# Kernel tuning notes

Measured on AMD Instinct MI355X. Metric: run time of the kernel, lower is better.

## Reference

```python
import jax, jax.numpy as jnp
import numpy as np

SC = 30.0
M = 0.5
EPS = 1e-12  # F.normalize default eps


def _l2norm(x, axis):
    n = jnp.sqrt(jnp.sum(x * x, axis=axis, keepdims=True))
    return x / jnp.maximum(n, EPS)


def setup_inputs() -> dict:
    key = jax.random.key(0)
    k1, k2, k3, k4, k5 = jax.random.split(key, 5)
    n, in_f, out_f, books, words = 1024, 2048, 4096, 8, 256
    lw = in_f // books  # len_word = 256
    # xavier_uniform-ish scale for params
    w_lim = np.sqrt(6.0 / (out_f + lw))
    m_lim = np.sqrt(6.0 / (lw + words))
    return {
        "input": jax.random.normal(k1, (n, in_f), dtype=jnp.float32),
        "label": jax.random.randint(k2, (n,), 0, out_f, dtype=jnp.int64),
        "weight": jax.random.uniform(k3, (books, out_f, lw), jnp.float32, -w_lim, w_lim),
        "mlp": jax.random.uniform(k4, (books, lw, words), jnp.float32, -m_lim, m_lim),
        "codebooks": jax.random.normal(k5, (books, lw, words), dtype=jnp.float32),
    }


def reference(input, label, weight, mlp, codebooks):
    n, in_f = input.shape
    books, out_f, lw = weight.shape
    # split input into per-book chunks: [books, n, lw]
    x = input.reshape(n, books, lw).transpose(1, 0, 2)
    wn = _l2norm(weight, axis=2)               # [books, out_f, lw]
    xn = _l2norm(x, axis=2)                    # [books, n, lw]
    cos_xw = jnp.clip(jnp.einsum('bnd,bod->bno', xn, wn), -1.0, 1.0)  # [books,n,out_f]
    # per-book soft codeword assignment
    xc_soft = jax.nn.softmax(jnp.einsum('bnd,bdw->bnw', x, mlp), axis=2)  # [books,n,words]
    # soft-quantized features s_m: codebooks @ xc_soft^T -> [books, lw, n] -> [books, n, lw]
    s = jnp.einsum('bdw,bnw->bnd', codebooks, xc_soft)
    sn = _l2norm(s, axis=2)
    cos_sw = jnp.clip(jnp.einsum('bnd,bod->bno', sn, wn), -1.0, 1.0)
    # margin one-hot combine: oh*(cos - m) + (1-oh)*cos == cos - oh*m
    oh = jax.nn.one_hot(label, out_f, dtype=cos_xw.dtype)[None]  # [1, n, out_f]
    out1 = SC * (cos_xw - oh * M)
    out2 = SC * (cos_sw - oh * M)
    return (out1.transpose(1, 0, 2), out2.transpose(1, 0, 2), xc_soft.transpose(1, 0, 2))
```

## Files before the change

kernel.cpp:

```cpp
#include <hip/hip_runtime.h>

typedef __attribute__((ext_vector_type(8))) short short8;
typedef __attribute__((ext_vector_type(4))) float f32x4;
typedef __attribute__((ext_vector_type(8))) unsigned short u16x8;

#define BOOKS 8
#define NSAMP 1024
#define OUTF  4096
#define KDIM  256
#define OUT2_OFF 33554432ull
#define OUT3_OFF 67108864ull

__device__ __forceinline__ unsigned short f2bf(float f) {
  unsigned int u = __float_as_uint(f);
  u += 0x7fffu + ((u >> 16) & 1u);
  return (unsigned short)(u >> 16);
}

__device__ __forceinline__ float wave_sum(float v) {
  #pragma unroll
  for (int off = 32; off; off >>= 1) v += __shfl_xor(v, off, 64);
  return v;
}
__device__ __forceinline__ float wave_max(float v) {
  #pragma unroll
  for (int off = 32; off; off >>= 1) v = fmaxf(v, __shfl_xor(v, off, 64));
  return v;
}

__global__ __launch_bounds__(256) void wnorm_kernel(const float* __restrict__ w,
                                                    unsigned short* __restrict__ wn) {
  int row  = blockIdx.x * 4 + (threadIdx.x >> 6);
  int lane = threadIdx.x & 63;
  float4 v = ((const float4*)(w + (size_t)row * KDIM))[lane];
  float ss = wave_sum(v.x*v.x + v.y*v.y + v.z*v.z + v.w*v.w);
  float inv = 1.f / fmaxf(sqrtf(ss), 1e-12f);
  ushort4 o;
  o.x = f2bf(v.x*inv); o.y = f2bf(v.y*inv); o.z = f2bf(v.z*inv); o.w = f2bf(v.w*inv);
  *(ushort4*)(wn + (size_t)row * KDIM + lane * 4) = o;
}

__global__ __launch_bounds__(256) void prep_small_kernel(const float* __restrict__ mlp,
                                                         const float* __restrict__ cb,
                                                         unsigned short* __restrict__ mlpT,
                                                         unsigned short* __restrict__ cbb) {
  int blk = blockIdx.x;
  int b = blk >> 8, d = blk & 255;
  int w = threadIdx.x;
  size_t src = ((size_t)(b * 256 + d)) * 256 + w;
  cbb[src] = f2bf(cb[src]);
  mlpT[((size_t)b * 256 + w) * 256 + d] = f2bf(mlp[src]);
}

__global__ __launch_bounds__(256) void xprep_kernel(const float* __restrict__ input,
                                                    unsigned short* __restrict__ Xb,
                                                    unsigned short* __restrict__ An) {
  int id = blockIdx.x * 4 + (threadIdx.x >> 6);
  int b = id >> 10, i = id & 1023;
  int lane = threadIdx.x & 63;
  float4 v = ((const float4*)(input + (size_t)i * 2048 + b * 256))[lane];
  float ss = wave_sum(v.x*v.x + v.y*v.y + v.z*v.z + v.w*v.w);
  float inv = 1.f / fmaxf(sqrtf(ss), 1e-12f);
  ushort4 r;
  r.x = f2bf(v.x); r.y = f2bf(v.y); r.z = f2bf(v.z); r.w = f2bf(v.w);
  *(ushort4*)(Xb + (size_t)id * KDIM + lane * 4) = r;
  ushort4 n;
  n.x = f2bf(v.x*inv); n.y = f2bf(v.y*inv); n.z = f2bf(v.z*inv); n.w = f2bf(v.w*inv);
  *(ushort4*)(An + ((size_t)b * 2048 + i) * KDIM + lane * 4) = n;
}

__global__ __launch_bounds__(256) void softmax_kernel(const float* __restrict__ logits,
                                                      unsigned short* __restrict__ XCb,
                                                      float* __restrict__ out3) {
  int id = blockIdx.x * 4 + (threadIdx.x >> 6);
  int b = id >> 10, i = id & 1023;
  int lane = threadIdx.x & 63;
  float4 v = ((const float4*)(logits + (size_t)id * 256))[lane];
  float mx = wave_max(fmaxf(fmaxf(v.x, v.y), fmaxf(v.z, v.w)));
  float e0 = __expf(v.x - mx), e1 = __expf(v.y - mx), e2 = __expf(v.z - mx), e3 = __expf(v.w - mx);
  float s = wave_sum(e0 + e1 + e2 + e3);
  float inv = 1.f / s;
  ushort4 p;
  p.x = f2bf(e0*inv); p.y = f2bf(e1*inv); p.z = f2bf(e2*inv); p.w = f2bf(e3*inv);
  *(ushort4*)(XCb + (size_t)id * 256 + lane * 4) = p;
  float4 pf = make_float4(e0*inv, e1*inv, e2*inv, e3*inv);
  *(float4*)(out3 + ((size_t)i * 8 + b) * 256 + lane * 4) = pf;
}

__global__ __launch_bounds__(256) void snorm_kernel(const float* __restrict__ s,
                                                    unsigned short* __restrict__ An) {
  int id = blockIdx.x * 4 + (threadIdx.x >> 6);
  int b = id >> 10, i = id & 1023;
  int lane = threadIdx.x & 63;
  float4 v = ((const float4*)(s + (size_t)id * 256))[lane];
  float ss = wave_sum(v.x*v.x + v.y*v.y + v.z*v.z + v.w*v.w);
  float inv = 1.f / fmaxf(sqrtf(ss), 1e-12f);
  ushort4 n;
  n.x = f2bf(v.x*inv); n.y = f2bf(v.y*inv); n.z = f2bf(v.z*inv); n.w = f2bf(v.w*inv);
  *(ushort4*)(An + ((size_t)b * 2048 + 1024 + i) * KDIM + lane * 4) = n;
}

template <int EPI>
__global__ __launch_bounds__(256) void gemm_bt_kernel(const unsigned short* __restrict__ A,
                                                      const unsigned short* __restrict__ B,
                                                      float* __restrict__ Cf,
                                                      const int* __restrict__ label,
                                                      int M, int N, int K) {
  __shared__ __align__(16) unsigned short lA[128 * 32];
  __shared__ __align__(16) unsigned short lB[128 * 32];

  const int b  = blockIdx.z;
  const int m0 = blockIdx.y * 128;
  const int n0 = blockIdx.x * 128;
  const int tid  = threadIdx.x;
  const int wid  = tid >> 6;
  const int lane = tid & 63;
  const int wm = wid & 1, wn = wid >> 1;
  const int r16 = lane & 15;
  const int q   = lane >> 4;

  const unsigned short* Ab = A + (size_t)b * M * K;
  const unsigned short* Bb = B + (size_t)b * N * K;

  f32x4 acc[4][4];
  #pragma unroll
  for (int i = 0; i < 4; ++i)
    #pragma unroll
    for (int j = 0; j < 4; ++j) acc[i][j] = (f32x4){0.f, 0.f, 0.f, 0.f};

  for (int k0 = 0; k0 < K; k0 += 32) {
    u16x8 ra[2], rb[2];
    #pragma unroll
    for (int c = 0; c < 2; ++c) {
      int idx = c * 256 + tid;
      int row = idx >> 2, ko = (idx & 3) * 8;
      ra[c] = *(const u16x8*)(Ab + (size_t)(m0 + row) * K + k0 + ko);
      rb[c] = *(const u16x8*)(Bb + (size_t)(n0 + row) * K + k0 + ko);
    }
    __syncthreads();
    #pragma unroll
    for (int c = 0; c < 2; ++c) {
      int idx = c * 256 + tid;
      int row = idx >> 2, ko = (idx & 3) * 8;
      *(u16x8*)(lA + row * 32 + ko) = ra[c];
      *(u16x8*)(lB + row * 32 + ko) = rb[c];
    }
    __syncthreads();

    short8 af[4], bfr[4];
    #pragma unroll
    for (int f = 0; f < 4; ++f) {
      af[f]  = *(const short8*)(lA + (wm * 64 + f * 16 + r16) * 32 + q * 8);
      bfr[f] = *(const short8*)(lB + (wn * 64 + f * 16 + r16) * 32 + q * 8);
    }
    #pragma unroll
    for (int i = 0; i < 4; ++i)
      #pragma unroll
      for (int j = 0; j < 4; ++j)
        acc[i][j] = __builtin_amdgcn_mfma_f32_16x16x32_bf16(af[i], bfr[j], acc[i][j], 0, 0, 0);
  }

  if constexpr (EPI == 0) {
    float* Cb = Cf + (size_t)b * M * N;
    #pragma unroll
    for (int i = 0; i < 4; ++i) {
      int row = m0 + wm * 64 + i * 16 + q * 4;
      #pragma unroll
      for (int j = 0; j < 4; ++j) {
        int col = n0 + wn * 64 + j * 16 + r16;
        #pragma unroll
        for (int r = 0; r < 4; ++r) Cb[(size_t)(row + r) * N + col] = acc[i][j][r];
      }
    }
  } else {
    #pragma unroll
    for (int i = 0; i < 4; ++i) {
      int row0 = m0 + wm * 64 + i * 16 + q * 4;
      #pragma unroll
      for (int r = 0; r < 4; ++r) {
        int row = row0 + r;
        int gi  = row & 1023;
        int lb  = label[gi];
        size_t base = (size_t)(row >> 10) * OUT2_OFF + ((size_t)gi * 8 + b) * OUTF;
        #pragma unroll
        for (int j = 0; j < 4; ++j) {
          int col = n0 + wn * 64 + j * 16 + r16;
          float v = fminf(fmaxf(acc[i][j][r], -1.f), 1.f) * 30.f;
          if (col == lb) v -= 15.f;
          Cf[base + col] = v;
        }
      }
    }
  }
}

extern "C" void kernel_launch(void* const* d_in, const int* in_sizes, int n_in,
                              void* d_out, int out_size, void* d_ws, size_t ws_size,
                              hipStream_t stream) {
  const float* input  = (const float*)d_in[0];
  const int*   label  = (const int*)d_in[1];
  const float* weight = (const float*)d_in[2];
  const float* mlp    = (const float*)d_in[3];
  const float* cb     = (const float*)d_in[4];
  float* out = (float*)d_out;

  unsigned short* wn = (unsigned short*)d_ws;
  unsigned short* An = wn + 8388608;

  float*          fbuf = out;
  unsigned short* Xb   = (unsigned short*)(out + OUT2_OFF);
  unsigned short* mlpT = Xb + 2097152;
  unsigned short* cbb  = mlpT + 524288;
  float*          out3 = out + OUT3_OFF;

  wnorm_kernel<<<dim3(8192), dim3(256), 0, stream>>>(weight, wn);
  prep_small_kernel<<<dim3(2048), dim3(256), 0, stream>>>(mlp, cb, mlpT, cbb);
  xprep_kernel<<<dim3(2048), dim3(256), 0, stream>>>(input, Xb, An);
  gemm_bt_kernel<0><<<dim3(2, 8, 8), dim3(256), 0, stream>>>(Xb, mlpT, fbuf, nullptr,
                                                             1024, 256, 256);
  softmax_kernel<<<dim3(2048), dim3(256), 0, stream>>>(fbuf, Xb, out3);
  gemm_bt_kernel<0><<<dim3(2, 8, 8), dim3(256), 0, stream>>>(Xb, cbb, fbuf, nullptr,
                                                             1024, 256, 256);
  snorm_kernel<<<dim3(2048), dim3(256), 0, stream>>>(fbuf, An);
  gemm_bt_kernel<1><<<dim3(32, 16, 8), dim3(256), 0, stream>>>(An, wn, out, label,
                                                               2048, 4096, 256);
}
```

Before: 402.9 us.

## Fuse soft-assignment GEMM, softmax, codebook GEMM and normalize into one kernel

Replaces the two small GEMMs plus separate softmax and s-normalization kernels with a single mid_kernel. Each block computes a 64-row tile of logits, applies the softmax in registers, stages the probabilities in swizzled LDS, and feeds them directly into the codebook GEMM before normalizing and writing An. This removes the fp32 round trips through global memory and three launches. The big GEMM also switches to global_load_lds direct-to-LDS loads. A cost is that the fused kernel runs only 128 blocks, which limits parallelism across the device.

```diff
diff --git a/kernel.cpp b/kernel.cpp
--- a/kernel.cpp
+++ b/kernel.cpp
@@ -16,16 +16,30 @@
   u += 0x7fffu + ((u >> 16) & 1u);
   return (unsigned short)(u >> 16);
 }
+__device__ __forceinline__ float b2f(unsigned short u) {
+  return __uint_as_float((unsigned)u << 16);
+}
 
 __device__ __forceinline__ float wave_sum(float v) {
   #pragma unroll
   for (int off = 32; off; off >>= 1) v += __shfl_xor(v, off, 64);
   return v;
 }
-__device__ __forceinline__ float wave_max(float v) {
-  #pragma unroll
-  for (int off = 32; off; off >>= 1) v = fmaxf(v, __shfl_xor(v, off, 64));
+__device__ __forceinline__ float qsum(float v) {
+  #pragma unroll
+  for (int off = 1; off < 16; off <<= 1) v += __shfl_xor(v, off, 64);
   return v;
+}
+__device__ __forceinline__ float qmax(float v) {
+  #pragma unroll
+  for (int off = 1; off < 16; off <<= 1) v = fmaxf(v, __shfl_xor(v, off, 64));
+  return v;
+}
+
+__device__ __forceinline__ void gll16(const void* g, void* l) {
+  __builtin_amdgcn_global_load_lds((const __attribute__((address_space(1))) void*)g,
+                                   (__attribute__((address_space(3))) void*)l,
+                                   16, 0, 0);
 }
 
 __global__ __launch_bounds__(256) void wnorm_kernel(const float* __restrict__ w,
@@ -69,43 +83,139 @@
   *(ushort4*)(An + ((size_t)b * 2048 + i) * KDIM + lane * 4) = n;
 }
 
-__global__ __launch_bounds__(256) void softmax_kernel(const float* __restrict__ logits,
-                                                      unsigned short* __restrict__ XCb,
-                                                      float* __restrict__ out3) {
-  int id = blockIdx.x * 4 + (threadIdx.x >> 6);
-  int b = id >> 10, i = id & 1023;
-  int lane = threadIdx.x & 63;
-  float4 v = ((const float4*)(logits + (size_t)id * 256))[lane];
-  float mx = wave_max(fmaxf(fmaxf(v.x, v.y), fmaxf(v.z, v.w)));
-  float e0 = __expf(v.x - mx), e1 = __expf(v.y - mx), e2 = __expf(v.z - mx), e3 = __expf(v.w - mx);
-  float s = wave_sum(e0 + e1 + e2 + e3);
-  float inv = 1.f / s;
-  ushort4 p;
-  p.x = f2bf(e0*inv); p.y = f2bf(e1*inv); p.z = f2bf(e2*inv); p.w = f2bf(e3*inv);
-  *(ushort4*)(XCb + (size_t)id * 256 + lane * 4) = p;
-  float4 pf = make_float4(e0*inv, e1*inv, e2*inv, e3*inv);
-  *(float4*)(out3 + ((size_t)i * 8 + b) * 256 + lane * 4) = pf;
-}
-
-__global__ __launch_bounds__(256) void snorm_kernel(const float* __restrict__ s,
-                                                    unsigned short* __restrict__ An) {
-  int id = blockIdx.x * 4 + (threadIdx.x >> 6);
-  int b = id >> 10, i = id & 1023;
-  int lane = threadIdx.x & 63;
-  float4 v = ((const float4*)(s + (size_t)id * 256))[lane];
-  float ss = wave_sum(v.x*v.x + v.y*v.y + v.z*v.z + v.w*v.w);
-  float inv = 1.f / fmaxf(sqrtf(ss), 1e-12f);
-  ushort4 n;
-  n.x = f2bf(v.x*inv); n.y = f2bf(v.y*inv); n.z = f2bf(v.z*inv); n.w = f2bf(v.w*inv);
-  *(ushort4*)(An + ((size_t)b * 2048 + 1024 + i) * KDIM + lane * 4) = n;
-}
-
-template <int EPI>
-__global__ __launch_bounds__(256) void gemm_bt_kernel(const unsigned short* __restrict__ A,
-                                                      const unsigned short* __restrict__ B,
-                                                      float* __restrict__ Cf,
-                                                      const int* __restrict__ label,
-                                                      int M, int N, int K) {
+__global__ __launch_bounds__(256) void mid_kernel(const unsigned short* __restrict__ Xb,
+                                                  const unsigned short* __restrict__ mlpT,
+                                                  const unsigned short* __restrict__ cbb,
+                                                  unsigned short* __restrict__ An,
+                                                  float* __restrict__ out3) {
+  __shared__ __align__(16) unsigned short lA[64 * 32];
+  __shared__ __align__(16) unsigned short lB[256 * 32];
+  __shared__ __align__(16) unsigned short lX[64 * 256];
+
+  const int b  = blockIdx.x >> 4;
+  const int m0 = (blockIdx.x & 15) * 64;
+  const int tid  = threadIdx.x;
+  const int wv   = tid >> 6;
+  const int lane = tid & 63;
+  const int r16  = lane & 15;
+  const int q    = lane >> 4;
+
+  const unsigned short* Ab = Xb   + ((size_t)b * NSAMP + m0) * KDIM;
+  const unsigned short* Bm = mlpT + (size_t)b * 256 * KDIM;
+  const unsigned short* Bc = cbb  + (size_t)b * 256 * KDIM;
+
+  f32x4 acc[16];
+  #pragma unroll
+  for (int j = 0; j < 16; ++j) acc[j] = (f32x4){0.f, 0.f, 0.f, 0.f};
+
+  for (int k0 = 0; k0 < KDIM; k0 += 32) {
+    __syncthreads();
+    { int row = tid >> 2, ko = (tid & 3) * 8;
+      gll16(Ab + (size_t)row * KDIM + k0 + ko, &lA[tid * 8]); }
+    #pragma unroll
+    for (int c = 0; c < 4; ++c) {
+      int idx = c * 256 + tid;
+      int row = idx >> 2, ko = (idx & 3) * 8;
+      gll16(Bm + (size_t)row * KDIM + k0 + ko, &lB[idx * 8]);
+    }
+    __syncthreads();
+    short8 af = *(const short8*)(lA + (wv * 16 + r16) * 32 + q * 8);
+    #pragma unroll
+    for (int j = 0; j < 16; ++j) {
+      short8 bf = *(const short8*)(lB + (j * 16 + r16) * 32 + q * 8);
+      acc[j] = __builtin_amdgcn_mfma_f32_16x16x32_bf16(af, bf, acc[j], 0, 0, 0);
+    }
+  }
+
+  #pragma unroll
+  for (int r = 0; r < 4; ++r) {
+    float mx = acc[0][r];
+    #pragma unroll
+    for (int j = 1; j < 16; ++j) mx = fmaxf(mx, acc[j][r]);
+    mx = qmax(mx);
+    float s = 0.f;
+    #pragma unroll
+    for (int j = 0; j < 16; ++j) { float e = __expf(acc[j][r] - mx); acc[j][r] = e; s += e; }
+    s = qsum(s);
+    float inv = 1.f / s;
+    int row = wv * 16 + q * 4 + r;
+    unsigned rb  = (unsigned)row * 512;
+    unsigned msk = ((unsigned)(row & 7)) << 4;
+    #pragma unroll
+    for (int j = 0; j < 16; ++j) {
+      unsigned byte = (rb + (unsigned)(j * 16 + r16) * 2) ^ msk;
+      *(unsigned short*)((char*)lX + byte) = f2bf(acc[j][r] * inv);
+    }
+  }
+  __syncthreads();
+
+  #pragma unroll
+  for (int p = 0; p < 8; ++p) {
+    int chunk = p * 256 + tid;
+    int row = chunk >> 5;
+    int c8  = (chunk & 31) * 8;
+    unsigned byte = ((unsigned)(row * 512 + c8 * 2)) ^ (((unsigned)(row & 7)) << 4);
+    u16x8 v = *(const u16x8*)((char*)lX + byte);
+    size_t o = ((size_t)(m0 + row) * 8 + b) * 256 + c8;
+    float4 f0 = make_float4(b2f(v[0]), b2f(v[1]), b2f(v[2]), b2f(v[3]));
+    float4 f1 = make_float4(b2f(v[4]), b2f(v[5]), b2f(v[6]), b2f(v[7]));
+    *(float4*)(out3 + o)     = f0;
+    *(float4*)(out3 + o + 4) = f1;
+  }
+
+  #pragma unroll
+  for (int j = 0; j < 16; ++j) acc[j] = (f32x4){0.f, 0.f, 0.f, 0.f};
+  for (int k0 = 0; k0 < KDIM; k0 += 32) {
+    __syncthreads();
+    #pragma unroll
+    for (int c = 0; c < 4; ++c) {
+      int idx = c * 256 + tid;
+      int row = idx >> 2, ko = (idx & 3) * 8;
+      gll16(Bc + (size_t)row * KDIM + k0 + ko, &lB[idx * 8]);
+    }
+    __syncthreads();
+    int arow = wv * 16 + r16;
+    unsigned abyte = ((unsigned)(arow * 512 + (k0 + q * 8) * 2)) ^ (((unsigned)(arow & 7)) << 4);
+    short8 af = *(const short8*)((char*)lX + abyte);
+    #pragma unroll
+    for (int j = 0; j < 16; ++j) {
+      short8 bf = *(const short8*)(lB + (j * 16 + r16) * 32 + q * 8);
+      acc[j] = __builtin_amdgcn_mfma_f32_16x16x32_bf16(af, bf, acc[j], 0, 0, 0);
+    }
+  }
+
+  #pragma unroll
+  for (int r = 0; r < 4; ++r) {
+    float ss = 0.f;
+    #pragma unroll
+    for (int j = 0; j < 16; ++j) ss += acc[j][r] * acc[j][r];
+    ss = qsum(ss);
+    float iv = 1.f / fmaxf(sqrtf(ss), 1e-12f);
+    int row = wv * 16 + q * 4 + r;
+    unsigned rb  = (unsigned)row * 512;
+    unsigned msk = ((unsigned)(row & 7)) << 4;
+    #pragma unroll
+    for (int j = 0; j < 16; ++j) {
+      unsigned byte = (rb + (unsigned)(j * 16 + r16) * 2) ^ msk;
+      *(unsigned short*)((char*)lX + byte) = f2bf(acc[j][r] * iv);
+    }
+  }
+  __syncthreads();
+  #pragma unroll
+  for (int p = 0; p < 8; ++p) {
+    int chunk = p * 256 + tid;
+    int row = chunk >> 5;
+    int c8  = (chunk & 31) * 8;
+    unsigned byte = ((unsigned)(row * 512 + c8 * 2)) ^ (((unsigned)(row & 7)) << 4);
+    u16x8 v = *(const u16x8*)((char*)lX + byte);
+    *(u16x8*)(An + ((size_t)b * 2048 + 1024 + m0 + row) * KDIM + c8) = v;
+  }
+}
+
+__global__ __launch_bounds__(256) void big_gemm_kernel(const unsigned short* __restrict__ A,
+                                                       const unsigned short* __restrict__ B,
+                                                       float* __restrict__ Cf,
+                                                       const int* __restrict__ label) {
   __shared__ __align__(16) unsigned short lA[128 * 32];
   __shared__ __align__(16) unsigned short lB[128 * 32];
 
@@ -119,8 +229,8 @@
   const int r16 = lane & 15;
   const int q   = lane >> 4;
 
-  const unsigned short* Ab = A + (size_t)b * M * K;
-  const unsigned short* Bb = B + (size_t)b * N * K;
+  const unsigned short* Ab = A + (size_t)b * 2048 * KDIM;
+  const unsigned short* Bb = B + (size_t)b * OUTF * KDIM;
 
   f32x4 acc[4][4];
   #pragma unroll
@@ -128,22 +238,14 @@
     #pragma unroll
     for (int j = 0; j < 4; ++j) acc[i][j] = (f32x4){0.f, 0.f, 0.f, 0.f};
 
-  for (int k0 = 0; k0 < K; k0 += 32) {
-    u16x8 ra[2], rb[2];
+  for (int k0 = 0; k0 < KDIM; k0 += 32) {
+    __syncthreads();
     #pragma unroll
     for (int c = 0; c < 2; ++c) {
       int idx = c * 256 + tid;
       int row = idx >> 2, ko = (idx & 3) * 8;
-      ra[c] = *(const u16x8*)(Ab + (size_t)(m0 + row) * K + k0 + ko);
-      rb[c] = *(const u16x8*)(Bb + (size_t)(n0 + row) * K + k0 + ko);
-    }
-    __syncthreads();
-    #pragma unroll
-    for (int c = 0; c < 2; ++c) {
-      int idx = c * 256 + tid;
-      int row = idx >> 2, ko = (idx & 3) * 8;
-      *(u16x8*)(lA + row * 32 + ko) = ra[c];
-      *(u16x8*)(lB + row * 32 + ko) = rb[c];
+      gll16(Ab + (size_t)(m0 + row) * KDIM + k0 + ko, &lA[idx * 8]);
+      gll16(Bb + (size_t)(n0 + row) * KDIM + k0 + ko, &lB[idx * 8]);
     }
     __syncthreads();
 
@@ -160,35 +262,21 @@
         acc[i][j] = __builtin_amdgcn_mfma_f32_16x16x32_bf16(af[i], bfr[j], acc[i][j], 0, 0, 0);
   }
 
-  if constexpr (EPI == 0) {
-    float* Cb = Cf + (size_t)b * M * N;
-    #pragma unroll
-    for (int i = 0; i < 4; ++i) {
-      int row = m0 + wm * 64 + i * 16 + q * 4;
+  #pragma unroll
+  for (int i = 0; i < 4; ++i) {
+    int row0 = m0 + wm * 64 + i * 16 + q * 4;
+    #pragma unroll
+    for (int r = 0; r < 4; ++r) {
+      int row = row0 + r;
+      int gi  = row & 1023;
+      int lb  = label[gi];
+      size_t base = (size_t)(row >> 10) * OUT2_OFF + ((size_t)gi * 8 + b) * OUTF;
       #pragma unroll
       for (int j = 0; j < 4; ++j) {
         int col = n0 + wn * 64 + j * 16 + r16;
-        #pragma unroll
-        for (int r = 0; r < 4; ++r) Cb[(size_t)(row + r) * N + col] = acc[i][j][r];
-      }
-    }
-  } else {
-    #pragma unroll
-    for (int i = 0; i < 4; ++i) {
-      int row0 = m0 + wm * 64 + i * 16 + q * 4;
-      #pragma unroll
-      for (int r = 0; r < 4; ++r) {
-        int row = row0 + r;
-        int gi  = row & 1023;
-        int lb  = label[gi];
-        size_t base = (size_t)(row >> 10) * OUT2_OFF + ((size_t)gi * 8 + b) * OUTF;
-        #pragma unroll
-        for (int j = 0; j < 4; ++j) {
-          int col = n0 + wn * 64 + j * 16 + r16;
-          float v = fminf(fmaxf(acc[i][j][r], -1.f), 1.f) * 30.f;
-          if (col == lb) v -= 15.f;
-          Cf[base + col] = v;
-        }
+        float v = fminf(fmaxf(acc[i][j][r], -1.f), 1.f) * 30.f;
+        if (col == lb) v -= 15.f;
+        Cf[base + col] = v;
       }
     }
   }
@@ -207,7 +295,6 @@
   unsigned short* wn = (unsigned short*)d_ws;
   unsigned short* An = wn + 8388608;
 
-  float*          fbuf = out;
   unsigned short* Xb   = (unsigned short*)(out + OUT2_OFF);
   unsigned short* mlpT = Xb + 2097152;
   unsigned short* cbb  = mlpT + 524288;
@@ -216,12 +303,6 @@
   wnorm_kernel<<<dim3(8192), dim3(256), 0, stream>>>(weight, wn);
   prep_small_kernel<<<dim3(2048), dim3(256), 0, stream>>>(mlp, cb, mlpT, cbb);
   xprep_kernel<<<dim3(2048), dim3(256), 0, stream>>>(input, Xb, An);
-  gemm_bt_kernel<0><<<dim3(2, 8, 8), dim3(256), 0, stream>>>(Xb, mlpT, fbuf, nullptr,
-                                                             1024, 256, 256);
-  softmax_kernel<<<dim3(2048), dim3(256), 0, stream>>>(fbuf, Xb, out3);
-  gemm_bt_kernel<0><<<dim3(2, 8, 8), dim3(256), 0, stream>>>(Xb, cbb, fbuf, nullptr,
-                                                             1024, 256, 256);
-  snorm_kernel<<<dim3(2048), dim3(256), 0, stream>>>(fbuf, An);
-  gemm_bt_kernel<1><<<dim3(32, 16, 8), dim3(256), 0, stream>>>(An, wn, out, label,
-                                                               2048, 4096, 256);
-}
+  mid_kernel<<<dim3(128), dim3(256), 0, stream>>>(Xb, mlpT, cbb, An, out3);
+  big_gemm_kernel<<<dim3(32, 16, 8), dim3(256), 0, stream>>>(An, wn, out, label);
+}
```

Result: faster. 379.8 us (-5.7%).
